# Performance work log

Measured on AMD Instinct MI355X. Metric: run time of the kernel, lower is better.

Reference implementation:

```python
import jax, jax.numpy as jnp
import numpy as np

N = 50000
E = 800000
IN_C = 128
HID = 128
OUT_C = 64
HEADS = 8
HD1 = HID // HEADS   # 16 per-head dim, layer 1 (concat)
HD2 = OUT_C          # 64 per-head dim, layer 2 (concat=False, mean over heads)
NEG_SLOPE = 0.2


def setup_inputs() -> dict:
    key = jax.random.key(0)
    ks = jax.random.split(key, 12)
    x = jax.random.normal(ks[0], (N, IN_C), dtype=jnp.float32)
    edge_index = jax.random.randint(ks[1], (2, E), 0, N, dtype=jnp.int64)
    s1 = 1.0 / np.sqrt(IN_C)
    s2 = 1.0 / np.sqrt(HID)
    W1 = jax.random.normal(ks[2], (IN_C, HEADS * HD1), dtype=jnp.float32) * s1
    att_src1 = jax.random.normal(ks[3], (HEADS, HD1), dtype=jnp.float32) * s1
    att_dst1 = jax.random.normal(ks[4], (HEADS, HD1), dtype=jnp.float32) * s1
    b1 = jnp.zeros((HID,), dtype=jnp.float32)
    W2 = jax.random.normal(ks[5], (HID, HEADS * HD2), dtype=jnp.float32) * s2
    att_src2 = jax.random.normal(ks[6], (HEADS, HD2), dtype=jnp.float32) * s2
    att_dst2 = jax.random.normal(ks[7], (HEADS, HD2), dtype=jnp.float32) * s2
    b2 = jnp.zeros((OUT_C,), dtype=jnp.float32)
    return {"x": x, "edge_index": edge_index,
            "W1": W1, "att_src1": att_src1, "att_dst1": att_dst1, "b1": b1,
            "W2": W2, "att_src2": att_src2, "att_dst2": att_dst2, "b2": b2}


def _gat_conv(x, W, a_src, a_dst, bias, src, dst, heads, head_dim, concat):
    n = x.shape[0]
    h = (x @ W).reshape(n, heads, head_dim)                      # [N,H,D]
    alpha_s = jnp.einsum('nhd,hd->nh', h, a_src)                  # [N,H]
    alpha_d = jnp.einsum('nhd,hd->nh', h, a_dst)                  # [N,H]
    e = jax.nn.leaky_relu(alpha_s[src] + alpha_d[dst], NEG_SLOPE)  # [E,H]
    # segment softmax over edges grouped by destination node
    m = jax.ops.segment_max(e, dst, num_segments=n)               # [N,H]
    m = jnp.where(jnp.isfinite(m), m, 0.0)
    ex = jnp.exp(e - m[dst])
    denom = jax.ops.segment_sum(ex, dst, num_segments=n)
    alpha = ex / (denom[dst] + 1e-16)                             # [E,H]
    out = jax.ops.segment_sum(h[src] * alpha[:, :, None], dst, num_segments=n)  # [N,H,D]
    if concat:
        out = out.reshape(n, heads * head_dim)
    else:
        out = out.mean(axis=1)
    return out + bias


def reference(x, edge_index, W1, att_src1, att_dst1, b1, W2, att_src2, att_dst2, b2):
    # PyG GATConv default add_self_loops=True
    loops = jnp.arange(N, dtype=edge_index.dtype)
    src = jnp.concatenate([edge_index[0], loops])
    dst = jnp.concatenate([edge_index[1], loops])
    h = _gat_conv(x, W1, att_src1, att_dst1, b1, src, dst, HEADS, HD1, True)
    h = jax.nn.relu(h)
    out = _gat_conv(h, W2, att_src2, att_dst2, b2, src, dst, HEADS, HD2, False)
    return out
```

## Files before the change

### kernel.cpp

```cpp
#include <hip/hip_runtime.h>

#define N_NODES 50000
#define N_EDGES 800000
#define ET (N_EDGES + N_NODES)
#define HEADS 8
#define NPAD 50048
#define SCAN_NB 196
#define CAP 96
#define LRS 1032
#define NB_DEG 3321
#define NB_GEMM1 782

typedef __attribute__((ext_vector_type(8))) _Float16 half8;
typedef __attribute__((ext_vector_type(2))) _Float16 half2v;
typedef __attribute__((ext_vector_type(4))) float f32x4;

__device__ __forceinline__ void wave_lds_fence(){
  asm volatile("s_waitcnt lgkmcnt(0)" ::: "memory");
}

__device__ __forceinline__ int edge_src(const int* ei, int e, int is64){
  if (e >= N_EDGES) return e - N_EDGES;
  return is64 ? ei[2*e] : ei[e];
}
__device__ __forceinline__ int edge_dst(const int* ei, int e, int is64){
  if (e >= N_EDGES) return e - N_EDGES;
  return is64 ? ei[2*(N_EDGES + e)] : ei[N_EDGES + e];
}

__global__ void k_init_wprep(const int* __restrict__ ei, int* __restrict__ deg,
                             int* __restrict__ cnt, int* __restrict__ flag,
                             const float* __restrict__ W1, const float* __restrict__ W2,
                             const float* __restrict__ as2, const float* __restrict__ ad2,
                             _Float16* __restrict__ Bp1, _Float16* __restrict__ Bp,
                             float* __restrict__ ws2, float* __restrict__ wd2){
  int b = blockIdx.x;
  int t_ = threadIdx.x;
  if (b < SCAN_NB){
    int i = b*256 + t_;
    if (i < N_NODES){ deg[i] = 0; cnt[i] = 0; }
    if (i == 0){
      int zeros = 0;
      for (int k = 0; k < 64; k++){
        if (ei[2*k + 1] == 0) zeros++;
      }
      *flag = (zeros >= 60) ? 1 : 0;
    }
  } else if (b < SCAN_NB + 256){
    int t = (b - SCAN_NB)*256 + t_;
    int j = t & 7, lane = (t >> 3) & 63, nt = (t >> 9) & 3, kt = t >> 11;
    int k = kt*32 + (lane >> 4)*8 + j;
    int c = nt*16 + (lane & 15);
    int h = k >> 7, kk = k & 127;
    Bp[t] = (_Float16)(0.125f * W2[kk*512 + h*64 + c]);
  } else if (b < SCAN_NB + 320){
    int t = (b - SCAN_NB - 256)*256 + t_;
    int j = t & 7, lane = (t >> 3) & 63, nt = (t >> 9) & 7, kt = t >> 12;
    int k = kt*32 + (lane >> 4)*8 + j;
    int c = nt*16 + (lane & 15);
    Bp1[t] = (_Float16)W1[k*128 + c];
  } else {
    int t = (b - SCAN_NB - 320)*256 + t_;
    int k = t >> 3, h = t & 7;
    float s = 0.f, d = 0.f;
    for (int dd = 0; dd < 64; dd++){
      float w = W2[k*512 + h*64 + dd];
      s += w * as2[h*64 + dd];
      d += w * ad2[h*64 + dd];
    }
    ws2[h*128 + k] = s;
    wd2[h*128 + k] = d;
  }
}

__global__ void __launch_bounds__(256) k_deg_gemm1(
    const int* __restrict__ ei, int* __restrict__ deg, const int* __restrict__ flag,
    const float* __restrict__ x, const _Float16* __restrict__ Bp1,
    _Float16* __restrict__ h1,
    const float* __restrict__ as1, const float* __restrict__ ad1,
    float* __restrict__ als1, float* __restrict__ ald1){
  if (blockIdx.x < NB_DEG){
    int e = blockIdx.x*blockDim.x + threadIdx.x;
    if (e >= ET) return;
    int is64 = *flag;
    int d = edge_dst(ei, e, is64);
    atomicAdd(&deg[d], 1);
    return;
  }
  int bid = blockIdx.x - NB_DEG;
  int tid = threadIdx.x;
  int lane = tid & 63, wv = tid >> 6;
  int n0 = bid*64 + wv*16;
  int rowA = n0 + (lane & 15);
  int koff = (lane >> 4)*8;
  const float* xr = x + (size_t)rowA*128 + koff;
  f32x4 acc[8];
  #pragma unroll
  for (int i = 0; i < 8; i++) acc[i] = (f32x4){0.f,0.f,0.f,0.f};
  bool inb = (rowA < N_NODES);
  #pragma unroll
  for (int kt = 0; kt < 4; kt++){
    half8 af;
    if (inb){
      float4 a0 = *(const float4*)(xr + kt*32);
      float4 a1 = *(const float4*)(xr + kt*32 + 4);
      af = (half8){(_Float16)a0.x,(_Float16)a0.y,(_Float16)a0.z,(_Float16)a0.w,
                   (_Float16)a1.x,(_Float16)a1.y,(_Float16)a1.z,(_Float16)a1.w};
    } else {
      af = (half8){0,0,0,0,0,0,0,0};
    }
    #pragma unroll
    for (int nt = 0; nt < 8; nt++){
      half8 bf = *(const half8*)(Bp1 + (((kt*8 + nt)*64 + lane) << 3));
      acc[nt] = __builtin_amdgcn_mfma_f32_16x16x32_f16(af, bf, acc[nt], 0, 0, 0);
    }
  }
  int m = lane & 15, q = lane >> 4;
  int r0 = n0 + q*4;
  #pragma unroll
  for (int nt = 0; nt < 8; nt++){
    int c = nt*16 + m;
    #pragma unroll
    for (int r = 0; r < 4; r++){
      int n = r0 + r;
      if (n < N_NODES) h1[(size_t)n*128 + c] = (_Float16)acc[nt][r];
    }
  }
  float as1v[8], ad1v[8];
  #pragma unroll
  for (int nt = 0; nt < 8; nt++){
    as1v[nt] = as1[nt*16 + m];
    ad1v[nt] = ad1[nt*16 + m];
  }
  #pragma unroll
  for (int r = 0; r < 4; r++){
    float vs[8], vd[8];
    #pragma unroll
    for (int nt = 0; nt < 8; nt++){
      vs[nt] = acc[nt][r]*as1v[nt];
      vd[nt] = acc[nt][r]*ad1v[nt];
      #pragma unroll
      for (int off = 1; off < 16; off <<= 1){
        vs[nt] += __shfl_xor(vs[nt], off, 64);
        vd[nt] += __shfl_xor(vd[nt], off, 64);
      }
    }
    int n = r0 + r;
    if (m == r && n < N_NODES){
      float4 v0; v0.x = vs[0]; v0.y = vs[1]; v0.z = vs[2]; v0.w = vs[3];
      float4 v1; v1.x = vs[4]; v1.y = vs[5]; v1.z = vs[6]; v1.w = vs[7];
      float4 w0; w0.x = vd[0]; w0.y = vd[1]; w0.z = vd[2]; w0.w = vd[3];
      float4 w1; w1.x = vd[4]; w1.y = vd[5]; w1.z = vd[6]; w1.w = vd[7];
      *(float4*)&als1[n*8]     = v0;
      *(float4*)&als1[n*8 + 4] = v1;
      *(float4*)&ald1[n*8]     = w0;
      *(float4*)&ald1[n*8 + 4] = w1;
    }
  }
}

__global__ void k_scan_part(const int* __restrict__ deg, int* __restrict__ loc,
                            int* __restrict__ part){
  __shared__ int lds[256];
  int t = threadIdx.x, i = blockIdx.x*256 + t;
  int v = (i < N_NODES) ? deg[i] : 0;
  lds[t] = v;
  __syncthreads();
  for (int off = 1; off < 256; off <<= 1){
    int x = (t >= off) ? lds[t - off] : 0;
    __syncthreads();
    lds[t] += x;
    __syncthreads();
  }
  if (i < N_NODES) loc[i] = lds[t] - v;
  if (t == 255) part[blockIdx.x] = lds[255];
}

__global__ void k_scan_carry(int* __restrict__ part, int* __restrict__ carry){
  __shared__ int lds[256];
  int t = threadIdx.x;
  int v = (t < SCAN_NB) ? part[t] : 0;
  lds[t] = v;
  __syncthreads();
  for (int off = 1; off < 256; off <<= 1){
    int x = (t >= off) ? lds[t - off] : 0;
    __syncthreads();
    lds[t] += x;
    __syncthreads();
  }
  if (t < SCAN_NB) carry[t] = lds[t] - v;
}

__global__ void k_scan_add(const int* __restrict__ loc, const int* __restrict__ carry,
                           int* __restrict__ row_ptr){
  int i = blockIdx.x*blockDim.x + threadIdx.x;
  if (i < N_NODES) row_ptr[i] = loc[i] + carry[i >> 8];
  if (i == 0) row_ptr[N_NODES] = ET;
}

__global__ void k_fill(const int* __restrict__ ei, const int* __restrict__ row_ptr,
                       int* __restrict__ cnt, int* __restrict__ col,
                       const int* __restrict__ flag,
                       const float* __restrict__ als1, const float* __restrict__ ald1,
                       _Float16* __restrict__ ew1){
  int e = blockIdx.x*blockDim.x + threadIdx.x;
  if (e >= ET) return;
  int is64 = *flag;
  int s = edge_src(ei, e, is64);
  int d = edge_dst(ei, e, is64);
  int pos = atomicAdd(&cnt[d], 1);
  int slot = row_ptr[d] + pos;
  col[slot] = s;
  float4 a0 = *(const float4*)(als1 + (size_t)s*8);
  float4 a1 = *(const float4*)(als1 + (size_t)s*8 + 4);
  float4 d0 = *(const float4*)(ald1 + (size_t)d*8);
  float4 d1 = *(const float4*)(ald1 + (size_t)d*8 + 4);
  float av[8] = {a0.x+d0.x, a0.y+d0.y, a0.z+d0.z, a0.w+d0.w,
                 a1.x+d1.x, a1.y+d1.y, a1.z+d1.z, a1.w+d1.w};
  half8 w;
  #pragma unroll
  for (int h = 0; h < 8; h++){
    float a = av[h];
    a = (a > 0.f) ? a : 0.2f*a;
    w[h] = (_Float16)__expf(a);
  }
  *(half8*)(ew1 + (size_t)slot*8) = w;
}

__global__ void k_attn_agg1(const _Float16* __restrict__ h1,
    const _Float16* __restrict__ ew1,
    const int* __restrict__ row_ptr, const int* __restrict__ col,
    const float* __restrict__ bias, _Float16* __restrict__ hr,
    const float* __restrict__ ws2, const float* __restrict__ wd2,
    float* __restrict__ als2, float* __restrict__ ald2){
  __shared__ _Float16 ew_s[4][CAP*8];
  __shared__ int col_s[4][CAP];
  __shared__ _Float16 ot_s[4][136];
  int tid = threadIdx.x;
  int wv = tid >> 6, lane = tid & 63;
  int n = blockIdx.x*4 + wv;
  int beg = row_ptr[n], end = row_ptr[n+1];
  int deg = end - beg;
  int items = deg*8;
  _Float16* es = ew_s[wv];
  int* cs = col_s[wv];
  const _Float16* ewr = ew1 + (size_t)beg*8;
  float l = 0.f;
  int itc = items < CAP*8 ? items : CAP*8;
  int it = lane;
  for (; it < itc; it += 64){
    _Float16 w = ewr[it];
    es[it] = w;
    l += (float)w;
    if ((it & 7) == 0) cs[it >> 3] = col[beg + (it >> 3)];
  }
  for (; it < items; it += 64){
    l += (float)ewr[it];
  }
  l += __shfl_xor(l, 8, 64);
  l += __shfl_xor(l, 16, 64);
  l += __shfl_xor(l, 32, 64);
  float inv = 1.f / (l + 1e-16f);
  wave_lds_fence();
  int eg = lane >> 4, cb = lane & 15;
  int hq = cb >> 1;
  float invh = __shfl(inv, hq, 64);
  float acc[8];
  #pragma unroll
  for (int k = 0; k < 8; k++) acc[k] = 0.f;
  int degc = deg < CAP ? deg : CAP;
  int j = 0;
  for (; j + 3 < degc; j += 4){
    int e = j + eg;
    int s = cs[e];
    float w = (float)es[e*8 + hq] * invh;
    half8 v = *(const half8*)(h1 + (size_t)s*128 + cb*8);
    #pragma unroll
    for (int k = 0; k < 8; k++) acc[k] += w*(float)v[k];
  }
  if (j < degc){
    int e = j + eg;
    if (e < degc){
      int s = cs[e];
      float w = (float)es[e*8 + hq] * invh;
      half8 v = *(const half8*)(h1 + (size_t)s*128 + cb*8);
      #pragma unroll
      for (int k = 0; k < 8; k++) acc[k] += w*(float)v[k];
    }
  }
  for (int jj = degc; jj < deg; jj += 4){
    int e = jj + eg;
    if (e < deg){
      int s = col[beg + e];
      float w = (float)ewr[e*8 + hq] * invh;
      half8 v = *(const half8*)(h1 + (size_t)s*128 + cb*8);
      #pragma unroll
      for (int k = 0; k < 8; k++) acc[k] += w*(float)v[k];
    }
  }
  #pragma unroll
  for (int k = 0; k < 8; k++){
    acc[k] += __shfl_xor(acc[k], 16, 64);
    acc[k] += __shfl_xor(acc[k], 32, 64);
  }
  float4 b0 = *(const float4*)(bias + cb*8);
  float4 b1 = *(const float4*)(bias + cb*8 + 4);
  float bb[8] = {b0.x,b0.y,b0.z,b0.w,b1.x,b1.y,b1.z,b1.w};
  half8 oh;
  #pragma unroll
  for (int k = 0; k < 8; k++) oh[k] = (_Float16)fmaxf(acc[k] + bb[k], 0.f);
  if (eg == 0){
    *(half8*)(hr + (size_t)n*128 + cb*8) = oh;
    ((half8*)&ot_s[wv][0])[cb] = oh;
  }
  wave_lds_fence();
  int hh = lane >> 3, seg = lane & 7;
  const half2v* otp = (const half2v*)&ot_s[wv][0];
  const float* wsr = ws2 + hh*128 + seg*16;
  const float* wdr = wd2 + hh*128 + seg*16;
  float vs = 0.f, vd = 0.f;
  #pragma unroll
  for (int i = 0; i < 8; i++){
    half2v v = otp[seg*8 + i];
    float vx = (float)v.x, vy = (float)v.y;
    vs += vx*wsr[2*i] + vy*wsr[2*i + 1];
    vd += vx*wdr[2*i] + vy*wdr[2*i + 1];
  }
  vs += __shfl_xor(vs, 1, 64); vd += __shfl_xor(vd, 1, 64);
  vs += __shfl_xor(vs, 2, 64); vd += __shfl_xor(vd, 2, 64);
  vs += __shfl_xor(vs, 4, 64); vd += __shfl_xor(vd, 4, 64);
  if (seg == 0){
    als2[n*8 + hh] = vs;
    ald2[n*8 + hh] = vd;
  }
}

__global__ void __launch_bounds__(1024) k_attn_agg2(const _Float16* __restrict__ hr,
    const float* __restrict__ als, const float* __restrict__ ald,
    const int* __restrict__ row_ptr, const int* __restrict__ col,
    const _Float16* __restrict__ Bp, const float* __restrict__ b2,
    float* __restrict__ outp){
  __shared__ _Float16 ew_s[16][CAP*8];
  __shared__ int col_s[16][CAP];
  __shared__ _Float16 at[16*LRS];
  int tid = threadIdx.x;
  int wv = tid >> 6, lane = tid & 63;
  int n = blockIdx.x*16 + wv;
  int beg = row_ptr[n], end = row_ptr[n+1];
  int deg = end - beg;
  int items = deg*8;
  int h = lane & 7;
  float ad = ald[n*8 + h];
  _Float16* es = ew_s[wv];
  int* cs = col_s[wv];
  float l = 0.f;
  int itc = items < CAP*8 ? items : CAP*8;
  int it = lane;
  for (; it < itc; it += 64){
    int e = it >> 3;
    int s = col[beg + e];
    float a = als[s*8 + h] + ad;
    a = (a > 0.f) ? a : 0.2f*a;
    float ex = __expf(a);
    es[it] = (_Float16)ex;
    if ((it & 7) == 0) cs[e] = s;
    l += ex;
  }
  for (; it < items; it += 64){
    int s = col[beg + (it >> 3)];
    float a = als[s*8 + h] + ad;
    a = (a > 0.f) ? a : 0.2f*a;
    l += __expf(a);
  }
  l += __shfl_xor(l, 8, 64);
  l += __shfl_xor(l, 16, 64);
  l += __shfl_xor(l, 32, 64);
  float inv = 1.f / (l + 1e-16f);
  wave_lds_fence();
  int hp = lane >> 4, cb = lane & 15;
  float invA = __shfl(inv, 2*hp, 64);
  float invB = __shfl(inv, 2*hp + 1, 64);
  half2v inv2; inv2.x = (_Float16)invA; inv2.y = (_Float16)invB;
  half2v acc_a[4], acc_b[4];
  #pragma unroll
  for (int i = 0; i < 4; i++){
    acc_a[i] = (half2v){(_Float16)0.f, (_Float16)0.f};
    acc_b[i] = (half2v){(_Float16)0.f, (_Float16)0.f};
  }
  int degc = deg < CAP ? deg : CAP;
  const _Float16* esw = es + 2*hp;
  int j = 0;
  half8 cv0, cv1, cv2, cv3;
  if (j + 3 < degc){
    cv0 = *(const half8*)(hr + (size_t)cs[j+0]*128 + cb*8);
    cv1 = *(const half8*)(hr + (size_t)cs[j+1]*128 + cb*8);
    cv2 = *(const half8*)(hr + (size_t)cs[j+2]*128 + cb*8);
    cv3 = *(const half8*)(hr + (size_t)cs[j+3]*128 + cb*8);
  }
  for (; j + 7 < degc; j += 4){
    half8 nv0 = *(const half8*)(hr + (size_t)cs[j+4]*128 + cb*8);
    half8 nv1 = *(const half8*)(hr + (size_t)cs[j+5]*128 + cb*8);
    half8 nv2 = *(const half8*)(hr + (size_t)cs[j+6]*128 + cb*8);
    half8 nv3 = *(const half8*)(hr + (size_t)cs[j+7]*128 + cb*8);
    half2v w0 = *(const half2v*)(esw + (j+0)*8) * inv2;
    half2v w1 = *(const half2v*)(esw + (j+1)*8) * inv2;
    half2v w2 = *(const half2v*)(esw + (j+2)*8) * inv2;
    half2v w3 = *(const half2v*)(esw + (j+3)*8) * inv2;
    #pragma unroll
    for (int k = 0; k < 4; k++){
      half2v t;
      t = (half2v){cv0[2*k], cv0[2*k+1]};
      acc_a[k] += (half2v){w0.x, w0.x} * t;
      acc_b[k] += (half2v){w0.y, w0.y} * t;
      t = (half2v){cv1[2*k], cv1[2*k+1]};
      acc_a[k] += (half2v){w1.x, w1.x} * t;
      acc_b[k] += (half2v){w1.y, w1.y} * t;
      t = (half2v){cv2[2*k], cv2[2*k+1]};
      acc_a[k] += (half2v){w2.x, w2.x} * t;
      acc_b[k] += (half2v){w2.y, w2.y} * t;
      t = (half2v){cv3[2*k], cv3[2*k+1]};
      acc_a[k] += (half2v){w3.x, w3.x} * t;
      acc_b[k] += (half2v){w3.y, w3.y} * t;
    }
    cv0 = nv0; cv1 = nv1; cv2 = nv2; cv3 = nv3;
  }
  if (j + 3 < degc){
    half2v w0 = *(const half2v*)(esw + (j+0)*8) * inv2;
    half2v w1 = *(const half2v*)(esw + (j+1)*8) * inv2;
    half2v w2 = *(const half2v*)(esw + (j+2)*8) * inv2;
    half2v w3 = *(const half2v*)(esw + (j+3)*8) * inv2;
    #pragma unroll
    for (int k = 0; k < 4; k++){
      half2v t;
      t = (half2v){cv0[2*k], cv0[2*k+1]};
      acc_a[k] += (half2v){w0.x, w0.x} * t;
      acc_b[k] += (half2v){w0.y, w0.y} * t;
      t = (half2v){cv1[2*k], cv1[2*k+1]};
      acc_a[k] += (half2v){w1.x, w1.x} * t;
      acc_b[k] += (half2v){w1.y, w1.y} * t;
      t = (half2v){cv2[2*k], cv2[2*k+1]};
      acc_a[k] += (half2v){w2.x, w2.x} * t;
      acc_b[k] += (half2v){w2.y, w2.y} * t;
      t = (half2v){cv3[2*k], cv3[2*k+1]};
      acc_a[k] += (half2v){w3.x, w3.x} * t;
      acc_b[k] += (half2v){w3.y, w3.y} * t;
    }
    j += 4;
  }
  for (; j < degc; j++){
    int s = cs[j];
    half2v w = *(const half2v*)(esw + j*8) * inv2;
    half8 v = *(const half8*)(hr + (size_t)s*128 + cb*8);
    #pragma unroll
    for (int k = 0; k < 4; k++){
      half2v t = (half2v){v[2*k], v[2*k+1]};
      acc_a[k] += (half2v){w.x, w.x} * t;
      acc_b[k] += (half2v){w.y, w.y} * t;
    }
  }
  if (deg > CAP){
    float2 adv = *(const float2*)(ald + (size_t)n*8 + 2*hp);
    for (; j < deg; j++){
      int s = col[beg + j];
      float2 alv = *(const float2*)(als + (size_t)s*8 + 2*hp);
      float a0 = alv.x + adv.x; a0 = (a0 > 0.f) ? a0 : 0.2f*a0;
      float a1 = alv.y + adv.y; a1 = (a1 > 0.f) ? a1 : 0.2f*a1;
      _Float16 w0 = (_Float16)(__expf(a0)*invA);
      _Float16 w1 = (_Float16)(__expf(a1)*invB);
      half8 v = *(const half8*)(hr + (size_t)s*128 + cb*8);
      #pragma unroll
      for (int k = 0; k < 4; k++){
        half2v t = (half2v){v[2*k], v[2*k+1]};
        acc_a[k] += (half2v){w0, w0} * t;
        acc_b[k] += (half2v){w1, w1} * t;
      }
    }
  }
  _Float16* ar = at + wv*LRS + (2*hp)*128 + cb*8;
  half8 oa, ob;
  #pragma unroll
  for (int k = 0; k < 4; k++){
    oa[2*k] = acc_a[k].x; oa[2*k+1] = acc_a[k].y;
    ob[2*k] = acc_b[k].x; ob[2*k+1] = acc_b[k].y;
  }
  *(half8*)ar = oa;
  *(half8*)(ar + 128) = ob;
  __syncthreads();
  if (wv >= 4) return;
  int m = lane & 15, q = lane >> 4;
  const _Float16* arow = at + m*LRS + q*8;
  f32x4 cacc = (f32x4){0.f,0.f,0.f,0.f};
  #pragma unroll 4
  for (int kt = 0; kt < 32; kt++){
    half8 af = *(const half8*)(arow + kt*32);
    half8 bf = *(const half8*)(Bp + (((kt*4 + wv)*64 + lane) << 3));
    cacc = __builtin_amdgcn_mfma_f32_16x16x32_f16(af, bf, cacc, 0, 0, 0);
  }
  int c = wv*16 + m;
  float bb = b2[c];
  #pragma unroll
  for (int r = 0; r < 4; r++){
    int nrow = blockIdx.x*16 + q*4 + r;
    outp[(size_t)nrow*64 + c] = cacc[r] + bb;
  }
}

extern "C" void kernel_launch(void* const* d_in, const int* in_sizes, int n_in,
                              void* d_out, int out_size, void* d_ws, size_t ws_size,
                              hipStream_t stream){
  const float* x   = (const float*)d_in[0];
  const int*   ei  = (const int*)d_in[1];
  const float* W1  = (const float*)d_in[2];
  const float* as1 = (const float*)d_in[3];
  const float* ad1 = (const float*)d_in[4];
  const float* b1  = (const float*)d_in[5];
  const float* W2  = (const float*)d_in[6];
  const float* as2 = (const float*)d_in[7];
  const float* ad2 = (const float*)d_in[8];
  const float* b2  = (const float*)d_in[9];
  float* outp = (float*)d_out;

  char* p = (char*)d_ws;
  auto alloc = [&](size_t bytes) -> void* {
    void* r = (void*)p;
    p += (bytes + 255) & ~(size_t)255;
    return r;
  };
  _Float16* h1  = (_Float16*)alloc((size_t)NPAD*128*2);
  _Float16* hr  = (_Float16*)alloc((size_t)N_NODES*128*2);
  _Float16* ew1 = (_Float16*)alloc((size_t)ET*8*2);
  float* als1 = (float*)alloc((size_t)N_NODES*8*4);
  float* ald1 = (float*)alloc((size_t)N_NODES*8*4);
  float* als2 = (float*)alloc((size_t)N_NODES*8*4);
  float* ald2 = (float*)alloc((size_t)N_NODES*8*4);
  int* row_ptr = (int*)alloc((size_t)(N_NODES+1)*4);
  int* deg  = (int*)alloc((size_t)N_NODES*4);
  int* cnt  = (int*)alloc((size_t)N_NODES*4);
  int* col  = (int*)alloc((size_t)ET*4);
  int* loc  = (int*)alloc((size_t)N_NODES*4);
  int* part = (int*)alloc(256*4);
  int* carry= (int*)alloc(256*4);
  int* flag = (int*)alloc(256);
  float* ws2 = (float*)alloc(1024*4);
  float* wd2 = (float*)alloc(1024*4);
  _Float16* Bp1 = (_Float16*)alloc((size_t)16384*2);
  _Float16* Bp  = (_Float16*)alloc((size_t)65536*2);

  dim3 b256(256);
  k_init_wprep<<<SCAN_NB + 324, b256, 0, stream>>>(ei, deg, cnt, flag,
                                                   W1, W2, as2, ad2,
                                                   Bp1, Bp, ws2, wd2);
  k_deg_gemm1<<<NB_DEG + NB_GEMM1, b256, 0, stream>>>(ei, deg, flag,
                                                      x, Bp1, h1, as1, ad1,
                                                      als1, ald1);
  k_scan_part<<<SCAN_NB, b256, 0, stream>>>(deg, loc, part);
  k_scan_carry<<<1, b256, 0, stream>>>(part, carry);
  k_scan_add<<<SCAN_NB, b256, 0, stream>>>(loc, carry, row_ptr);
  k_fill<<<(ET+255)/256, b256, 0, stream>>>(ei, row_ptr, cnt, col, flag,
                                            als1, ald1, ew1);
  k_attn_agg1<<<N_NODES/4, b256, 0, stream>>>(h1, ew1, row_ptr, col,
                                              b1, hr, ws2, wd2, als2, ald2);
  k_attn_agg2<<<N_NODES/16, dim3(1024), 0, stream>>>(hr, als2, ald2, row_ptr, col,
                                                     Bp, b2, outp);
}
```

Measured before the change: 322.3 us.

## Precompute layer-2 edge attention weights in a separate edge-parallel kernel

Adds a k_fill output recording the destination per CSR slot and a new edge-parallel kernel that computes the layer-2 exp(leaky_relu) weights into an fp16 buffer. k_attn_agg2 then reads those weights instead of gathering als2 per source and evaluating exp inline. This is meant to move the random gathers and transcendental work out of the latency-bound aggregation kernel into a fully parallel pass. In exchange it adds a kernel launch and extra global traffic: writing and reading ET*8 halves plus the new destination array.

```diff
diff --git a/kernel.cpp b/kernel.cpp
--- a/kernel.cpp
+++ b/kernel.cpp
@@ -202,7 +202,7 @@
                        int* __restrict__ cnt, int* __restrict__ col,
                        const int* __restrict__ flag,
                        const float* __restrict__ als1, const float* __restrict__ ald1,
-                       _Float16* __restrict__ ew1){
+                       _Float16* __restrict__ ew1, int* __restrict__ dstv){
   int e = blockIdx.x*blockDim.x + threadIdx.x;
   if (e >= ET) return;
   int is64 = *flag;
@@ -211,6 +211,7 @@
   int pos = atomicAdd(&cnt[d], 1);
   int slot = row_ptr[d] + pos;
   col[slot] = s;
+  dstv[slot] = d;
   float4 a0 = *(const float4*)(als1 + (size_t)s*8);
   float4 a1 = *(const float4*)(als1 + (size_t)s*8 + 4);
   float4 d0 = *(const float4*)(ald1 + (size_t)d*8);
@@ -225,6 +226,28 @@
     w[h] = (_Float16)__expf(a);
   }
   *(half8*)(ew1 + (size_t)slot*8) = w;
+}
+
+__global__ void k_ew2(const int* __restrict__ col, const int* __restrict__ dstv,
+                      const float* __restrict__ als2, const float* __restrict__ ald2,
+                      _Float16* __restrict__ ew2){
+  int e = blockIdx.x*blockDim.x + threadIdx.x;
+  if (e >= ET) return;
+  int s = col[e], d = dstv[e];
+  float4 a0 = *(const float4*)(als2 + (size_t)s*8);
+  float4 a1 = *(const float4*)(als2 + (size_t)s*8 + 4);
+  float4 d0 = *(const float4*)(ald2 + (size_t)d*8);
+  float4 d1 = *(const float4*)(ald2 + (size_t)d*8 + 4);
+  float av[8] = {a0.x+d0.x, a0.y+d0.y, a0.z+d0.z, a0.w+d0.w,
+                 a1.x+d1.x, a1.y+d1.y, a1.z+d1.z, a1.w+d1.w};
+  half8 w;
+  #pragma unroll
+  for (int h = 0; h < 8; h++){
+    float a = av[h];
+    a = (a > 0.f) ? a : 0.2f*a;
+    w[h] = (_Float16)__expf(a);
+  }
+  *(half8*)(ew2 + (size_t)e*8) = w;
 }
 
 __global__ void k_attn_agg1(const _Float16* __restrict__ h1,
@@ -336,7 +359,7 @@
 }
 
 __global__ void __launch_bounds__(1024) k_attn_agg2(const _Float16* __restrict__ hr,
-    const float* __restrict__ als, const float* __restrict__ ald,
+    const _Float16* __restrict__ ew2,
     const int* __restrict__ row_ptr, const int* __restrict__ col,
     const _Float16* __restrict__ Bp, const float* __restrict__ b2,
     float* __restrict__ outp){
@@ -349,28 +372,20 @@
   int beg = row_ptr[n], end = row_ptr[n+1];
   int deg = end - beg;
   int items = deg*8;
-  int h = lane & 7;
-  float ad = ald[n*8 + h];
   _Float16* es = ew_s[wv];
   int* cs = col_s[wv];
+  const _Float16* ewr = ew2 + (size_t)beg*8;
   float l = 0.f;
   int itc = items < CAP*8 ? items : CAP*8;
   int it = lane;
   for (; it < itc; it += 64){
-    int e = it >> 3;
-    int s = col[beg + e];
-    float a = als[s*8 + h] + ad;
-    a = (a > 0.f) ? a : 0.2f*a;
-    float ex = __expf(a);
-    es[it] = (_Float16)ex;
-    if ((it & 7) == 0) cs[e] = s;
-    l += ex;
+    _Float16 w = ewr[it];
+    es[it] = w;
+    l += (float)w;
+    if ((it & 7) == 0) cs[it >> 3] = col[beg + (it >> 3)];
   }
   for (; it < items; it += 64){
-    int s = col[beg + (it >> 3)];
-    float a = als[s*8 + h] + ad;
-    a = (a > 0.f) ? a : 0.2f*a;
-    l += __expf(a);
+    l += (float)ewr[it];
   }
   l += __shfl_xor(l, 8, 64);
   l += __shfl_xor(l, 16, 64);
@@ -459,20 +474,15 @@
     }
   }
   if (deg > CAP){
-    float2 adv = *(const float2*)(ald + (size_t)n*8 + 2*hp);
     for (; j < deg; j++){
       int s = col[beg + j];
-      float2 alv = *(const float2*)(als + (size_t)s*8 + 2*hp);
-      float a0 = alv.x + adv.x; a0 = (a0 > 0.f) ? a0 : 0.2f*a0;
-      float a1 = alv.y + adv.y; a1 = (a1 > 0.f) ? a1 : 0.2f*a1;
-      _Float16 w0 = (_Float16)(__expf(a0)*invA);
-      _Float16 w1 = (_Float16)(__expf(a1)*invB);
+      half2v w = *(const half2v*)(ewr + j*8 + 2*hp) * inv2;
       half8 v = *(const half8*)(hr + (size_t)s*128 + cb*8);
       #pragma unroll
       for (int k = 0; k < 4; k++){
         half2v t = (half2v){v[2*k], v[2*k+1]};
-        acc_a[k] += (half2v){w0, w0} * t;
-        acc_b[k] += (half2v){w1, w1} * t;
+        acc_a[k] += (half2v){w.x, w.x} * t;
+        acc_b[k] += (half2v){w.y, w.y} * t;
       }
     }
   }
@@ -529,6 +539,7 @@
   _Float16* h1  = (_Float16*)alloc((size_t)NPAD*128*2);
   _Float16* hr  = (_Float16*)alloc((size_t)N_NODES*128*2);
   _Float16* ew1 = (_Float16*)alloc((size_t)ET*8*2);
+  _Float16* ew2 = (_Float16*)alloc((size_t)ET*8*2);
   float* als1 = (float*)alloc((size_t)N_NODES*8*4);
   float* ald1 = (float*)alloc((size_t)N_NODES*8*4);
   float* als2 = (float*)alloc((size_t)N_NODES*8*4);
@@ -537,6 +548,7 @@
   int* deg  = (int*)alloc((size_t)N_NODES*4);
   int* cnt  = (int*)alloc((size_t)N_NODES*4);
   int* col  = (int*)alloc((size_t)ET*4);
+  int* dstv = (int*)alloc((size_t)ET*4);
   int* loc  = (int*)alloc((size_t)N_NODES*4);
   int* part = (int*)alloc(256*4);
   int* carry= (int*)alloc(256*4);
@@ -557,9 +569,10 @@
   k_scan_carry<<<1, b256, 0, stream>>>(part, carry);
   k_scan_add<<<SCAN_NB, b256, 0, stream>>>(loc, carry, row_ptr);
   k_fill<<<(ET+255)/256, b256, 0, stream>>>(ei, row_ptr, cnt, col, flag,
-                                            als1, ald1, ew1);
+                                            als1, ald1, ew1, dstv);
   k_attn_agg1<<<N_NODES/4, b256, 0, stream>>>(h1, ew1, row_ptr, col,
                                               b1, hr, ws2, wd2, als2, ald2);
-  k_attn_agg2<<<N_NODES/16, dim3(1024), 0, stream>>>(hr, als2, ald2, row_ptr, col,
+  k_ew2<<<NB_DEG, b256, 0, stream>>>(col, dstv, als2, ald2, ew2);
+  k_attn_agg2<<<N_NODES/16, dim3(1024), 0, stream>>>(hr, ew2, row_ptr, col,
                                                      Bp, b2, outp);
 }
```

Result: slower. 348.8 us (+8.2%).
